# Kernel optimization log

Hardware: AMD Instinct MI355X
Metric: run time of the kernel (lower is better)

## Reference

```python
import jax, jax.numpy as jnp
import numpy as np

D_MODEL = 1024
OMEGA_DIM = 64
VQ_CODES = 256
VQ_DIM = 64
N_PARAMS = OMEGA_DIM * (OMEGA_DIM - 1) // 2  # 2016
TRIU_R, TRIU_C = np.triu_indices(OMEGA_DIM, k=1)
RMS_EPS = 1e-6
NORM_EPS = 1e-12  # F.normalize default


def setup_inputs() -> dict:
    key = jax.random.key(0)
    ks = jax.random.split(key, 12)
    B, L = 16, 4096
    s = 0.02
    return {
        "x": jax.random.normal(ks[0], (B, L, D_MODEL), jnp.float32),
        "omega_proj_w": jax.random.normal(ks[1], (N_PARAMS, D_MODEL), jnp.float32) * s,
        "omega_proj_b": jnp.zeros((N_PARAMS,), jnp.float32),
        "omega_out_w": jax.random.normal(ks[2], (D_MODEL, OMEGA_DIM), jnp.float32) * s,
        "omega_out_b": jnp.zeros((D_MODEL,), jnp.float32),
        "vq_proj_in_w": jax.random.normal(ks[3], (VQ_DIM, D_MODEL), jnp.float32) * s,
        "vq_proj_in_b": jnp.zeros((VQ_DIM,), jnp.float32),
        "vq_proj_out_w": jax.random.normal(ks[4], (D_MODEL, VQ_DIM), jnp.float32) * s,
        "vq_proj_out_b": jnp.zeros((D_MODEL,), jnp.float32),
        "codebook": jax.random.normal(ks[5], (VQ_CODES, VQ_DIM), jnp.float32),
        "omega_mix": jnp.float32(0.1),
        "vq_mix": jnp.float32(0.05),
        "norm_w": jnp.ones((D_MODEL,), jnp.float32),
    }


def _normalize(v):
    n = jnp.linalg.norm(v, axis=-1, keepdims=True)
    return v / jnp.maximum(n, NORM_EPS)


def _rmsnorm(x, w):
    ms = jnp.mean(x * x, axis=-1, keepdims=True)
    return x * jax.lax.rsqrt(ms + RMS_EPS) * w


def reference(x, omega_proj_w, omega_proj_b, omega_out_w, omega_out_b,
              vq_proj_in_w, vq_proj_in_b, vq_proj_out_w, vq_proj_out_b,
              codebook, omega_mix, vq_mix, norm_w):
    B = x.shape[0]
    residual = x
    h_mean = jnp.mean(x, axis=1)  # [B, d_model]

    # --- Lie branch: skew-symmetric Omega -> Cayley (3rd-order Neumann) ---
    params = h_mean @ omega_proj_w.T + omega_proj_b  # [B, n_params]
    omega = jnp.zeros((B, OMEGA_DIM, OMEGA_DIM), x.dtype).at[:, TRIU_R, TRIU_C].set(params)
    omega = omega - jnp.swapaxes(omega, -1, -2)
    I = jnp.eye(OMEGA_DIM, dtype=x.dtype)
    omega2 = jnp.einsum('bij,bjk->bik', omega, omega)
    omega3 = jnp.einsum('bij,bjk->bik', omega2, omega)
    G = I + omega + 0.5 * omega2 + (1.0 / 6.0) * omega3  # [B, n, n]

    x_head = x[:, :, :OMEGA_DIM]
    x_rotated = jnp.einsum('bld,bde->ble', x_head, G)
    lie_out = x_rotated @ omega_out_w.T + omega_out_b  # [B, L, d_model]

    # --- VQ branch: cosine-sim codebook lookup with straight-through ---
    vq_input = h_mean @ vq_proj_in_w.T + vq_proj_in_b  # [B, vq_dim]
    scores = _normalize(vq_input) @ _normalize(codebook).T  # [B, vq_codes]
    vq_idx = jnp.argmax(scores, axis=-1)
    vq_code = codebook[vq_idx]  # [B, vq_dim]
    vq_out = vq_input + jax.lax.stop_gradient(vq_code - vq_input)
    vq_contribution = (vq_out @ vq_proj_out_w.T + vq_proj_out_b)[:, None, :]  # [B,1,d_model]

    out = residual + omega_mix * lie_out + vq_mix * vq_contribution
    return _rmsnorm(out, norm_w)
```

## Files before the change

### kernel.cpp

```cpp
#include <hip/hip_runtime.h>
#include <hip/hip_bf16.h>
#include <math.h>

#define BB 16
#define LL 4096
#define DD 1024
#define OD 64
#define NP 2016
#define NC 256
#define VD 64
#define NCHUNK 64
#define LCH (LL / NCHUNK)
#define TT 16
#define TPB 256
#define NROW (NP + VD)

typedef __attribute__((ext_vector_type(8))) short bf16x8;
typedef __attribute__((ext_vector_type(4))) float f32x4;

__device__ __forceinline__ int triu_idx(int r, int c) {
  return r * 63 - (r * (r - 1)) / 2 + (c - r - 1);
}
__device__ __forceinline__ unsigned short f2bf(float f) {
  unsigned int u = __float_as_uint(f);
  u += 0x7fffu + ((u >> 16) & 1u);
  return (unsigned short)(u >> 16);
}

__global__ void k_partial(const float* __restrict__ x, float* __restrict__ partial) {
  const int b = blockIdx.y, ch = blockIdx.x, tid = threadIdx.x;
  const float4* xp = (const float4*)(x + ((size_t)b * LL + (size_t)ch * LCH) * DD) + tid;
  float4 s = make_float4(0.f, 0.f, 0.f, 0.f);
  #pragma unroll 8
  for (int l = 0; l < LCH; ++l) {
    float4 v = xp[(size_t)l * (DD / 4)];
    s.x += v.x; s.y += v.y; s.z += v.z; s.w += v.w;
  }
  ((float4*)(partial + ((size_t)(b * NCHUNK + ch)) * DD))[tid] = s;
}

__global__ void k_mean(const float* __restrict__ partial, float* __restrict__ hm) {
  const int ch = blockIdx.x, b = blockIdx.y, tid = threadIdx.x;
  const int col = ch * 64 + (tid & 63), rg = tid >> 6;
  __shared__ float s_red[4][64];
  float s = 0.f;
  const float* pr = partial + (size_t)(b * NCHUNK + rg * 16) * DD + col;
  #pragma unroll
  for (int i = 0; i < 16; ++i) s += pr[(size_t)i * DD];
  s_red[rg][tid & 63] = s;
  __syncthreads();
  if (tid < 64) {
    const float v = s_red[0][tid] + s_red[1][tid] + s_red[2][tid] + s_red[3][tid];
    hm[(size_t)b * DD + ch * 64 + tid] = v * (1.f / (float)LL);
  }
}

__global__ void k_params(const float* __restrict__ hm,
                         const float* __restrict__ opw, const float* __restrict__ opb,
                         const float* __restrict__ viw, const float* __restrict__ vib,
                         float* __restrict__ params, float* __restrict__ vqi_g) {
  const int wave = threadIdx.x >> 6, lane = threadIdx.x & 63;
  const int p = blockIdx.x * 4 + wave;
  if (p >= NROW) return;
  const bool isvq = (p >= NP);
  const float* wr = isvq ? (viw + (size_t)(p - NP) * DD) : (opw + (size_t)p * DD);
  float acc[BB];
  #pragma unroll
  for (int b = 0; b < BB; ++b) acc[b] = 0.f;
  for (int i = 0; i < DD; i += 64) {
    const float wv = wr[i + lane];
    #pragma unroll
    for (int b = 0; b < BB; ++b) acc[b] = fmaf(wv, hm[b * DD + i + lane], acc[b]);
  }
  const float bias = isvq ? vib[p - NP] : opb[p];
  #pragma unroll
  for (int b = 0; b < BB; ++b) {
    float v = acc[b];
    #pragma unroll
    for (int mk = 32; mk; mk >>= 1) v += __shfl_xor(v, mk, 64);
    if (lane == 0) {
      if (isvq) vqi_g[(size_t)b * VD + (p - NP)] = v + bias;
      else      params[(size_t)b * NP + p] = v + bias;
    }
  }
}

__global__ __launch_bounds__(1024)
void k_perb(const float* __restrict__ params, const float* __restrict__ vqi_g,
            const float* __restrict__ cb,
            const float* __restrict__ oob, const float* __restrict__ vow,
            const float* __restrict__ vob,
            const float* __restrict__ omix_p, const float* __restrict__ vmix_p,
            float* __restrict__ Gout, float* __restrict__ cvec) {
  const int b = blockIdx.y, tid = threadIdx.x;
  if (blockIdx.x == 0) {
    __shared__ float om[OD][OD + 1];
    __shared__ float om2[OD][OD + 1];
    const float* par = params + (size_t)b * NP;
    #pragma unroll
    for (int q = 0; q < 4; ++q) {
      const int e2 = tid + q * 1024;
      const int i = e2 >> 6, j = e2 & 63;
      float v = 0.f;
      if (i < j) v = par[triu_idx(i, j)];
      else if (i > j) v = -par[triu_idx(j, i)];
      om[i][j] = v;
    }
    __syncthreads();
    #pragma unroll
    for (int q = 0; q < 4; ++q) {
      const int e2 = tid + q * 1024;
      const int i = e2 >> 6, j = e2 & 63;
      float s = 0.f;
      #pragma unroll 8
      for (int k = 0; k < OD; ++k) s = fmaf(om[i][k], om[k][j], s);
      om2[i][j] = s;
    }
    __syncthreads();
    #pragma unroll
    for (int q = 0; q < 4; ++q) {
      const int e2 = tid + q * 1024;
      const int i = e2 >> 6, j = e2 & 63;
      float s3 = 0.f;
      #pragma unroll 8
      for (int k = 0; k < OD; ++k) s3 = fmaf(om2[i][k], om[k][j], s3);
      Gout[(size_t)b * OD * OD + e2] =
          om[i][j] + 0.5f * om2[i][j] + (1.f / 6.f) * s3 + (i == j ? 1.f : 0.f);
    }
  } else {
    __shared__ float vq[VD];
    __shared__ float scb[NC];
    __shared__ int sib[NC];
    __shared__ float cd[VD];
    __shared__ float nv_s;
    if (tid < VD) vq[tid] = vqi_g[(size_t)b * VD + tid];
    __syncthreads();
    if (tid == 0) {
      float s = 0.f;
      for (int k = 0; k < VD; ++k) s += vq[k] * vq[k];
      nv_s = fmaxf(sqrtf(s), 1e-12f);
    }
    __syncthreads();
    if (tid < NC) {
      const float* cr = cb + (size_t)tid * VD;
      float dot = 0.f, ssq = 0.f;
      #pragma unroll 8
      for (int k = 0; k < VD; ++k) { float cv = cr[k]; dot = fmaf(cv, vq[k], dot); ssq = fmaf(cv, cv, ssq); }
      scb[tid] = dot / (nv_s * fmaxf(sqrtf(ssq), 1e-12f));
      sib[tid] = tid;
    }
    __syncthreads();
    for (int s2 = 128; s2 > 0; s2 >>= 1) {
      if (tid < s2) {
        float a = scb[tid], b2 = scb[tid + s2];
        int ia = sib[tid], ib = sib[tid + s2];
        if (b2 > a || (b2 == a && ib < ia)) { scb[tid] = b2; sib[tid] = ib; }
      }
      __syncthreads();
    }
    const int best = sib[0];
    if (tid < VD) cd[tid] = cb[(size_t)best * VD + tid];
    __syncthreads();
    const float omix = omix_p[0], vmix = vmix_p[0];
    {
      const int e = tid;
      float a = vob[e];
      const float* wr = vow + (size_t)e * VD;
      #pragma unroll 8
      for (int k = 0; k < VD; ++k) a = fmaf(cd[k], wr[k], a);
      cvec[(size_t)b * DD + e] = fmaf(omix, oob[e], vmix * a);
    }
  }
}

__global__ __launch_bounds__(1024)
void k_MTB(const float* __restrict__ G, const float* __restrict__ oow,
           const float* __restrict__ omix_p, unsigned short* __restrict__ MTB) {
  const int b = blockIdx.y, eb = blockIdx.x * 64, tid = threadIdx.x;
  __shared__ float g[OD][OD + 1];
  __shared__ float wl[64][65];
  #pragma unroll
  for (int q = 0; q < 4; ++q) {
    const int e2 = tid + q * 1024;
    g[e2 >> 6][e2 & 63] = G[(size_t)b * OD * OD + e2];
    wl[e2 >> 6][e2 & 63] = oow[(size_t)(eb + (e2 >> 6)) * 64 + (e2 & 63)];
  }
  __syncthreads();
  const float omix = omix_p[0];
  #pragma unroll
  for (int q = 0; q < 4; ++q) {
    const int o = tid + q * 1024;
    const int el = o >> 6, d = o & 63;
    float s = 0.f;
    #pragma unroll
    for (int k = 0; k < 64; ++k) s = fmaf(g[d][k], wl[el][k], s);
    MTB[((size_t)b * DD + eb + el) * OD + d] = f2bf(omix * s);
  }
}

#define STAGE_XH(BUF, TTOK)                                                          \
  if (stager) {                                                                      \
    const float4 v = *(const float4*)(x + xrow + (size_t)((TTOK) + stok) * DD + sd0);\
    unsigned int lo = (unsigned int)f2bf(v.x) | ((unsigned int)f2bf(v.y) << 16);     \
    unsigned int hi = (unsigned int)f2bf(v.z) | ((unsigned int)f2bf(v.w) << 16);     \
    *(uint2*)((char*)&(BUF)[0][0] + stok * 144 + sd0 * 2) = make_uint2(lo, hi);      \
  }

#define LOAD_RES(DST, TTOK)                                                          \
  _Pragma("unroll")                                                                  \
  for (int et = 0; et < 4; ++et) {                                                   \
    _Pragma("unroll")                                                                \
    for (int r = 0; r < 4; ++r)                                                      \
      DST[et][r] = x[xrow + (size_t)((TTOK) + g * 4 + r) * DD + ebase + et * 16 + c];\
  }

#define COMPUTE_TILE(XBUF, RES, PAR, TTOK)                                           \
  {                                                                                  \
    const char* xbB = (const char*)&(XBUF)[0][0];                                    \
    bf16x8 af0 = *(const bf16x8*)(xbB + c * 144 + g * 16);                           \
    bf16x8 af1 = *(const bf16x8*)(xbB + c * 144 + 64 + g * 16);                      \
    f32x4 acc[4];                                                                    \
    _Pragma("unroll")                                                                \
    for (int et = 0; et < 4; ++et) {                                                 \
      acc[et] = (f32x4){0.f, 0.f, 0.f, 0.f};                                         \
      acc[et] = __builtin_amdgcn_mfma_f32_16x16x32_bf16(af0, bf[et][0], acc[et], 0, 0, 0); \
      acc[et] = __builtin_amdgcn_mfma_f32_16x16x32_bf16(af1, bf[et][1], acc[et], 0, 0, 0); \
    }                                                                                \
    float pp[4] = {0.f, 0.f, 0.f, 0.f};                                              \
    _Pragma("unroll")                                                                \
    for (int et = 0; et < 4; ++et) {                                                 \
      _Pragma("unroll")                                                              \
      for (int r = 0; r < 4; ++r) {                                                  \
        const float y = RES[et][r] + acc[et][r] + ce_r[et];                          \
        acc[et][r] = y;                                                              \
        pp[r] = fmaf(y, y, pp[r]);                                                   \
      }                                                                              \
    }                                                                                \
    _Pragma("unroll")                                                                \
    for (int mk = 1; mk < 16; mk <<= 1) {                                            \
      _Pragma("unroll")                                                              \
      for (int r = 0; r < 4; ++r) pp[r] += __shfl_xor(pp[r], mk, 64);                \
    }                                                                                \
    if (c == 0) {                                                                    \
      _Pragma("unroll")                                                              \
      for (int r = 0; r < 4; ++r) red[PAR][g * 4 + r][w] = pp[r];                    \
    }                                                                                \
    __syncthreads();                                                                 \
    float sc_r[4];                                                                   \
    _Pragma("unroll")                                                                \
    for (int r = 0; r < 4; ++r) {                                                    \
      const float4* rp = (const float4*)&red[PAR][g * 4 + r][0];                     \
      const float4 s0 = rp[0], s1 = rp[1], s2 = rp[2], s3 = rp[3];                   \
      const float s = s0.x + s0.y + s0.z + s0.w + s1.x + s1.y + s1.z + s1.w          \
                    + s2.x + s2.y + s2.z + s2.w + s3.x + s3.y + s3.z + s3.w;         \
      sc_r[r] = rsqrtf(s * (1.f / (float)DD) + 1e-6f);                               \
    }                                                                                \
    _Pragma("unroll")                                                                \
    for (int et = 0; et < 4; ++et) {                                                 \
      _Pragma("unroll")                                                              \
      for (int r = 0; r < 4; ++r) {                                                  \
        out[xrow + (size_t)((TTOK) + g * 4 + r) * DD + ebase + et * 16 + c] =        \
            acc[et][r] * sc_r[r] * nw_r[et];                                         \
      }                                                                              \
    }                                                                                \
  }

__global__ __launch_bounds__(1024)
void k_mfma(const float* __restrict__ x, const unsigned short* __restrict__ MTB,
            const float* __restrict__ cvec, const float* __restrict__ nw,
            float* __restrict__ out) {
  const int b = blockIdx.y;
  const int Tblk = blockIdx.x * TPB;
  const int tid = threadIdx.x;
  const int w = tid >> 6, lane = tid & 63;
  const int c = lane & 15, g = lane >> 4;
  const int ebase = w * 64;

  __shared__ unsigned short xh[2][TT][72];
  __shared__ float red[2][TT][20];

  bf16x8 bf[4][2];
  {
    const unsigned short* mp = MTB + ((size_t)b * DD + ebase + c) * OD + g * 8;
    #pragma unroll
    for (int et = 0; et < 4; ++et) {
      #pragma unroll
      for (int ks = 0; ks < 2; ++ks)
        bf[et][ks] = *(const bf16x8*)(mp + (size_t)et * 16 * OD + ks * 32);
    }
  }
  float ce_r[4], nw_r[4];
  #pragma unroll
  for (int et = 0; et < 4; ++et) {
    ce_r[et] = cvec[(size_t)b * DD + ebase + et * 16 + c];
    nw_r[et] = nw[ebase + et * 16 + c];
  }

  const size_t xrow = ((size_t)b * LL + Tblk) * DD;
  const int stok = tid >> 4, sd0 = (tid & 15) * 4;
  const bool stager = (tid < 256);

  float resA[4][4], resB[4][4];

  STAGE_XH(xh[0], 0)
  LOAD_RES(resA, 0)
  __syncthreads();

  #pragma unroll 1
  for (int it = 0; it < TPB / (2 * TT); ++it) {
    const int te = it * 2 * TT;
    const int to = te + TT;
    const int tn = te + 2 * TT;
    STAGE_XH(xh[1], to)
    LOAD_RES(resB, to)
    COMPUTE_TILE(xh[0], resA, 0, te)
    if (it + 1 < TPB / (2 * TT)) {
      STAGE_XH(xh[0], tn)
      LOAD_RES(resA, tn)
    }
    COMPUTE_TILE(xh[1], resB, 1, to)
  }
}

extern "C" void kernel_launch(void* const* d_in, const int* in_sizes, int n_in,
                              void* d_out, int out_size, void* d_ws, size_t ws_size,
                              hipStream_t stream) {
  (void)in_sizes; (void)n_in; (void)out_size; (void)ws_size;
  const float* x    = (const float*)d_in[0];
  const float* opw  = (const float*)d_in[1];
  const float* opb  = (const float*)d_in[2];
  const float* oow  = (const float*)d_in[3];
  const float* oob  = (const float*)d_in[4];
  const float* viw  = (const float*)d_in[5];
  const float* vib  = (const float*)d_in[6];
  const float* vow  = (const float*)d_in[7];
  const float* vob  = (const float*)d_in[8];
  const float* cb   = (const float*)d_in[9];
  const float* omix = (const float*)d_in[10];
  const float* vmix = (const float*)d_in[11];
  const float* nw   = (const float*)d_in[12];
  float* out = (float*)d_out;

  float* ws      = (float*)d_ws;
  float* partial = ws;
  float* hm      = ws + 1048576;
  float* params  = ws + 1064960;
  float* vqi_g   = ws + 1097216;
  float* G       = ws + 1098240;
  unsigned short* MTB = (unsigned short*)(ws + 1163776);
  float* cvec    = ws + 1688064;

  k_partial<<<dim3(NCHUNK, BB), 256, 0, stream>>>(x, partial);
  k_mean<<<dim3(16, BB), 256, 0, stream>>>(partial, hm);
  k_params<<<NROW / 4, 256, 0, stream>>>(hm, opw, opb, viw, vib, params, vqi_g);
  k_perb<<<dim3(2, BB), 1024, 0, stream>>>(params, vqi_g, cb, oob, vow, vob,
                                           omix, vmix, G, cvec);
  k_MTB<<<dim3(16, BB), 1024, 0, stream>>>(G, oow, omix, MTB);
  k_mfma<<<dim3(LL / TPB, BB), 1024, 0, stream>>>(x, MTB, cvec, nw, out);
}
```

Before: 212.0 us.

## Fuse Cayley G computation into MTB kernel and use nontemporal output stores

Merges the per-batch G computation and the MTB projection into one kernel launch. Each of the 16 e-blocks per batch recomputes the Omega, Omega^2 and Omega^3 products itself instead of reading G from global memory. This removes a kernel launch and the G round-trip at the cost of 16x redundant small matmuls. The final output writes also become nontemporal stores to reduce cache pollution from the large streaming output.

```diff
diff --git a/kernel.cpp b/kernel.cpp
--- a/kernel.cpp
+++ b/kernel.cpp
@@ -86,16 +86,20 @@
 }
 
 __global__ __launch_bounds__(1024)
-void k_perb(const float* __restrict__ params, const float* __restrict__ vqi_g,
+void k_post(const float* __restrict__ params, const float* __restrict__ vqi_g,
             const float* __restrict__ cb,
             const float* __restrict__ oob, const float* __restrict__ vow,
             const float* __restrict__ vob,
             const float* __restrict__ omix_p, const float* __restrict__ vmix_p,
-            float* __restrict__ Gout, float* __restrict__ cvec) {
+            const float* __restrict__ oow,
+            unsigned short* __restrict__ MTB, float* __restrict__ cvec) {
   const int b = blockIdx.y, tid = threadIdx.x;
-  if (blockIdx.x == 0) {
+  const float omix = omix_p[0];
+  if (blockIdx.x < 16) {
     __shared__ float om[OD][OD + 1];
     __shared__ float om2[OD][OD + 1];
+    __shared__ float gs[OD][OD + 1];
+    const int eb = blockIdx.x * 64;
     const float* par = params + (size_t)b * NP;
     #pragma unroll
     for (int q = 0; q < 4; ++q) {
@@ -124,8 +128,24 @@
       float s3 = 0.f;
       #pragma unroll 8
       for (int k = 0; k < OD; ++k) s3 = fmaf(om2[i][k], om[k][j], s3);
-      Gout[(size_t)b * OD * OD + e2] =
-          om[i][j] + 0.5f * om2[i][j] + (1.f / 6.f) * s3 + (i == j ? 1.f : 0.f);
+      gs[i][j] = om[i][j] + 0.5f * om2[i][j] + (1.f / 6.f) * s3 + (i == j ? 1.f : 0.f);
+    }
+    __syncthreads();
+    float (*wl)[OD + 1] = om;
+    #pragma unroll
+    for (int q = 0; q < 4; ++q) {
+      const int e2 = tid + q * 1024;
+      wl[e2 >> 6][e2 & 63] = oow[(size_t)(eb + (e2 >> 6)) * 64 + (e2 & 63)];
+    }
+    __syncthreads();
+    #pragma unroll
+    for (int q = 0; q < 4; ++q) {
+      const int o = tid + q * 1024;
+      const int el = o >> 6, d = o & 63;
+      float s = 0.f;
+      #pragma unroll
+      for (int k = 0; k < 64; ++k) s = fmaf(gs[d][k], wl[el][k], s);
+      MTB[((size_t)b * DD + eb + el) * OD + d] = f2bf(omix * s);
     }
   } else {
     __shared__ float vq[VD];
@@ -161,7 +181,7 @@
     const int best = sib[0];
     if (tid < VD) cd[tid] = cb[(size_t)best * VD + tid];
     __syncthreads();
-    const float omix = omix_p[0], vmix = vmix_p[0];
+    const float vmix = vmix_p[0];
     {
       const int e = tid;
       float a = vob[e];
@@ -173,31 +193,6 @@
   }
 }
 
-__global__ __launch_bounds__(1024)
-void k_MTB(const float* __restrict__ G, const float* __restrict__ oow,
-           const float* __restrict__ omix_p, unsigned short* __restrict__ MTB) {
-  const int b = blockIdx.y, eb = blockIdx.x * 64, tid = threadIdx.x;
-  __shared__ float g[OD][OD + 1];
-  __shared__ float wl[64][65];
-  #pragma unroll
-  for (int q = 0; q < 4; ++q) {
-    const int e2 = tid + q * 1024;
-    g[e2 >> 6][e2 & 63] = G[(size_t)b * OD * OD + e2];
-    wl[e2 >> 6][e2 & 63] = oow[(size_t)(eb + (e2 >> 6)) * 64 + (e2 & 63)];
-  }
-  __syncthreads();
-  const float omix = omix_p[0];
-  #pragma unroll
-  for (int q = 0; q < 4; ++q) {
-    const int o = tid + q * 1024;
-    const int el = o >> 6, d = o & 63;
-    float s = 0.f;
-    #pragma unroll
-    for (int k = 0; k < 64; ++k) s = fmaf(g[d][k], wl[el][k], s);
-    MTB[((size_t)b * DD + eb + el) * OD + d] = f2bf(omix * s);
-  }
-}
-
 #define STAGE_XH(BUF, TTOK)                                                          \
   if (stager) {                                                                      \
     const float4 v = *(const float4*)(x + xrow + (size_t)((TTOK) + stok) * DD + sd0);\
@@ -259,8 +254,8 @@
     for (int et = 0; et < 4; ++et) {                                                 \
       _Pragma("unroll")                                                              \
       for (int r = 0; r < 4; ++r) {                                                  \
-        out[xrow + (size_t)((TTOK) + g * 4 + r) * DD + ebase + et * 16 + c] =        \
-            acc[et][r] * sc_r[r] * nw_r[et];                                         \
+        __builtin_nontemporal_store(acc[et][r] * sc_r[r] * nw_r[et],                 \
+            out + xrow + (size_t)((TTOK) + g * 4 + r) * DD + ebase + et * 16 + c);   \
       }                                                                              \
     }                                                                                \
   }
@@ -346,15 +341,13 @@
   float* hm      = ws + 1048576;
   float* params  = ws + 1064960;
   float* vqi_g   = ws + 1097216;
-  float* G       = ws + 1098240;
-  unsigned short* MTB = (unsigned short*)(ws + 1163776);
-  float* cvec    = ws + 1688064;
+  unsigned short* MTB = (unsigned short*)(ws + 1098240);
+  float* cvec    = ws + 1622528;
 
   k_partial<<<dim3(NCHUNK, BB), 256, 0, stream>>>(x, partial);
   k_mean<<<dim3(16, BB), 256, 0, stream>>>(partial, hm);
   k_params<<<NROW / 4, 256, 0, stream>>>(hm, opw, opb, viw, vib, params, vqi_g);
-  k_perb<<<dim3(2, BB), 1024, 0, stream>>>(params, vqi_g, cb, oob, vow, vob,
-                                           omix, vmix, G, cvec);
-  k_MTB<<<dim3(16, BB), 1024, 0, stream>>>(G, oow, omix, MTB);
+  k_post<<<dim3(17, BB), 1024, 0, stream>>>(params, vqi_g, cb, oob, vow, vob,
+                                            omix, vmix, oow, MTB, cvec);
   k_mfma<<<dim3(LL / TPB, BB), 1024, 0, stream>>>(x, MTB, cvec, nw, out);
 }
```

Measured after the change: 227.6 us. +7.4%, slower.
